# Kernel optimization log

Hardware: AMD Instinct MI355X
Metric: run time of the kernel (lower is better)

The kernel has to match this reference:

```python
import jax, jax.numpy as jnp
import numpy as np

B, S, D = 4, 2048, 768   # batch, seq_len, dim_inp
H, E = 12, 64            # num_heads, dim_out (per-head)
LN_EPS = 1e-5


def setup_inputs() -> dict:
    key = jax.random.key(0)
    ks = jax.random.split(key, 12)
    sd = 1.0 / np.sqrt(D)
    x = jax.random.normal(ks[0], (B, S, D), dtype=jnp.float32)
    Wq = jax.random.normal(ks[1], (H, D, E), dtype=jnp.float32) * sd
    bq = jax.random.normal(ks[2], (H, E), dtype=jnp.float32) * 0.02
    Wk = jax.random.normal(ks[3], (H, D, E), dtype=jnp.float32) * sd
    bk = jax.random.normal(ks[4], (H, E), dtype=jnp.float32) * 0.02
    Wv = jax.random.normal(ks[5], (H, D, E), dtype=jnp.float32) * sd
    bv = jax.random.normal(ks[6], (H, E), dtype=jnp.float32) * 0.02
    Wo = jax.random.normal(ks[7], (H * E, D), dtype=jnp.float32) * (1.0 / np.sqrt(H * E))
    bo = jax.random.normal(ks[8], (D,), dtype=jnp.float32) * 0.02
    gamma = jnp.ones((D,), dtype=jnp.float32)
    beta = jnp.zeros((D,), dtype=jnp.float32)
    return {"input_tensor": x, "Wq": Wq, "bq": bq, "Wk": Wk, "bk": bk,
            "Wv": Wv, "bv": bv, "Wo": Wo, "bo": bo, "gamma": gamma, "beta": beta}


def reference(input_tensor, Wq, bq, Wk, bk, Wv, bv, Wo, bo, gamma, beta):
    x = input_tensor  # [B,S,D]
    # all heads at once: [B,H,S,E]
    q = jnp.einsum('bsd,hde->bhse', x, Wq) + bq[None, :, None, :]
    k = jnp.einsum('bsd,hde->bhse', x, Wk) + bk[None, :, None, :]
    v = jnp.einsum('bsd,hde->bhse', x, Wv) + bv[None, :, None, :]
    # NOTE: original divides by sqrt(seq_len) (query.size(1)), not sqrt(head_dim)
    scale = jnp.sqrt(jnp.float32(q.shape[2]))
    scores = jnp.einsum('bhse,bhte->bhst', q, k) / scale  # [B,H,S,S]
    attn = jax.nn.softmax(scores, axis=-1)
    ctx = jnp.einsum('bhst,bhte->bhse', attn, v)          # [B,H,S,E]
    # concat heads along last dim: [B,S,H*E]
    ctx = ctx.transpose(0, 2, 1, 3).reshape(x.shape[0], x.shape[1], -1)
    proj = ctx @ Wo + bo                                   # [B,S,D]
    h = x + proj
    mu = jnp.mean(h, axis=-1, keepdims=True)
    var = jnp.mean(jnp.square(h - mu), axis=-1, keepdims=True)
    y = (h - mu) * jax.lax.rsqrt(var + LN_EPS) * gamma + beta
    return y
```

## Files before the change

kernel.cpp:

```cpp
#include <hip/hip_runtime.h>


typedef __bf16 bf16x8 __attribute__((ext_vector_type(8)));
typedef __bf16 bf16x4 __attribute__((ext_vector_type(4)));
typedef float  f32x4  __attribute__((ext_vector_type(4)));
typedef float  f32x16 __attribute__((ext_vector_type(16)));
typedef unsigned u32x4 __attribute__((ext_vector_type(4)));

#define MFMA16(a,b,c) __builtin_amdgcn_mfma_f32_16x16x32_bf16((a),(b),(c),0,0,0)
#define MFMA32(a,b,c) __builtin_amdgcn_mfma_f32_32x32x16_bf16((a),(b),(c),0,0,0)
#define QSCALE2 (0.022097086912079612f * 1.4426950408889634f)

__device__ __forceinline__ void gload16(const void* g, void* l) {
  __builtin_amdgcn_global_load_lds((const __attribute__((address_space(1))) void*)g,
                                   (__attribute__((address_space(3))) void*)l, 16, 0, 0);
}

__global__ __launch_bounds__(256) void pack_kernel(
    const float* __restrict__ x, const float* __restrict__ Wq,
    const float* __restrict__ Wk, const float* __restrict__ Wv,
    const float* __restrict__ Wo,
    __bf16* __restrict__ xb, __bf16* __restrict__ wqkv, __bf16* __restrict__ wot) {
  int tid = blockIdx.x * 256 + threadIdx.x;
  int nth = gridDim.x * 256;
  for (int i = tid; i < 8192 * 768 / 4; i += nth) {
    float4 v = ((const float4*)x)[i];
    bf16x4 o; o[0] = (__bf16)v.x; o[1] = (__bf16)v.y; o[2] = (__bf16)v.z; o[3] = (__bf16)v.w;
    ((bf16x4*)xb)[i] = o;
  }
  for (int i = tid; i < 3 * 768 * 768; i += nth) {
    int n = i / 768, d = i - n * 768;
    int p = n / 768;
    int wn = n - p * 768;
    int h = wn >> 6, e = wn & 63;
    const float* W = (p == 0) ? Wq : (p == 1) ? Wk : Wv;
    wqkv[i] = (__bf16)W[(h * 768 + d) * 64 + e];
  }
  for (int i = tid; i < 768 * 768; i += nth) {
    int n = i / 768, k = i - n * 768;
    wot[i] = (__bf16)Wo[k * 768 + n];
  }
}

#define GEMM_CORE(A_, Bt_, m0_, n0_)                                              \
  __shared__ __align__(16) __bf16 As[128 * 64];                                   \
  __shared__ __align__(16) __bf16 Bs[128 * 64];                                   \
  const int tid = threadIdx.x;                                                    \
  const int w = tid >> 6, lane = tid & 63, ln = lane & 15, hi = lane >> 4;        \
  const int wr = w >> 1, wc = w & 1;                                              \
  f32x4 acc[4][4];                                                                \
  {                                                                               \
    f32x4 z = {0.f, 0.f, 0.f, 0.f};                                               \
    _Pragma("unroll") for (int i = 0; i < 4; ++i)                                 \
      _Pragma("unroll") for (int j = 0; j < 4; ++j) acc[i][j] = z;                \
  }                                                                               \
  const int colx0 = ((hi) ^ (ln & 7)) << 4;         \
  const int colx1 = ((4 + hi) ^ (ln & 7)) << 4;     \
  {                                                                               \
    const int r0 = tid >> 3;                       \
    const int scb = ((tid & 7) * 16) ^ ((r0 & 7) << 4);     \
    const char* gA = (const char*)(A_) + (size_t)(m0_ + r0) * 1536 + scb;         \
    const char* gB = (const char*)(Bt_) + (size_t)(n0_ + r0) * 1536 + scb;        \
    char* lA = (char*)As + w * 1024;    \
    char* lB = (char*)Bs + w * 1024;                                              \
    for (int kt = 0; kt < 12; ++kt) {                                             \
      const int kb = kt * 128;                                                    \
      _Pragma("unroll") for (int j = 0; j < 4; ++j) {                             \
        gload16(gA + j * 49152 + kb, lA + j * 4096);                              \
        gload16(gB + j * 49152 + kb, lB + j * 4096);                              \
      }                                                                           \
      __syncthreads();                                                            \
      _Pragma("unroll") for (int kk = 0; kk < 2; ++kk) {                          \
        const int cx = kk ? colx1 : colx0;                                        \
        bf16x8 af[4], bfv[4];                                                     \
        _Pragma("unroll") for (int mt = 0; mt < 4; ++mt)                          \
          af[mt] = *(const bf16x8*)((char*)As + (wr * 64 + mt * 16 + ln) * 128 + cx); \
        _Pragma("unroll") for (int nt = 0; nt < 4; ++nt)                          \
          bfv[nt] = *(const bf16x8*)((char*)Bs + (wc * 64 + nt * 16 + ln) * 128 + cx); \
        _Pragma("unroll") for (int mt = 0; mt < 4; ++mt)                          \
          _Pragma("unroll") for (int nt = 0; nt < 4; ++nt)                        \
            acc[mt][nt] = MFMA16(af[mt], bfv[nt], acc[mt][nt]);                   \
      }                                                                           \
      __syncthreads();                                                            \
    }                                                                             \
  }

__global__ __launch_bounds__(256) void gemm_qkv(
    const __bf16* __restrict__ A, const __bf16* __restrict__ Bt,
    const float* __restrict__ bq, const float* __restrict__ bk,
    const float* __restrict__ bv,
    __bf16* __restrict__ qb, __bf16* __restrict__ kb, __bf16* __restrict__ vt) {
  const int lin = blockIdx.y * 18 + blockIdx.x;
  const int swzb = (lin & 7) * 144 + (lin >> 3);
  const int m0 = (swzb / 18) * 128, n0 = (swzb % 18) * 128;
  GEMM_CORE(A, Bt, m0, n0)
  const int p = n0 / 768;
  const float* bias = (p == 0) ? bq : (p == 1) ? bk : bv;
  const float sc = (p == 0) ? QSCALE2 : 1.0f;
#pragma unroll
  for (int nt = 0; nt < 4; ++nt) {
    int n = n0 + wc * 64 + nt * 16 + ln;
    int wn = n - p * 768;
    int h = wn >> 6, e = wn & 63;
    float bb = bias[wn];
#pragma unroll
    for (int mt = 0; mt < 4; ++mt) {
      int mrow = m0 + wr * 64 + mt * 16 + hi * 4;
      int b = mrow >> 11, s0 = mrow & 2047;
      if (p == 2) {
        bf16x4 pk;
#pragma unroll
        for (int r = 0; r < 4; ++r) pk[r] = (__bf16)(acc[mt][nt][r] + bb);
        *(bf16x4*)&vt[(((size_t)b * 12 + h) * 64 + e) * 2048 + s0] = pk;
      } else {
        __bf16* dst = (p == 0) ? qb : kb;
#pragma unroll
        for (int r = 0; r < 4; ++r)
          dst[(((size_t)b * 12 + h) * 2048 + s0 + r) * 64 + e] =
              (__bf16)((acc[mt][nt][r] + bb) * sc);
      }
    }
  }
}

__global__ __launch_bounds__(256) void gemm_proj(
    const __bf16* __restrict__ A, const __bf16* __restrict__ Bt,
    const float* __restrict__ bo, const __bf16* __restrict__ xres,
    __bf16* __restrict__ hout) {
  const int lin = blockIdx.y * 6 + blockIdx.x;
  const int swzb = (lin & 7) * 48 + (lin >> 3);
  const int m0 = (swzb / 6) * 128, n0 = (swzb % 6) * 128;
  GEMM_CORE(A, Bt, m0, n0)
#pragma unroll
  for (int nt = 0; nt < 4; ++nt) {
    int n = n0 + wc * 64 + nt * 16 + ln;
    float bb = bo[n];
#pragma unroll
    for (int mt = 0; mt < 4; ++mt) {
      int mrow = m0 + wr * 64 + mt * 16 + hi * 4;
#pragma unroll
      for (int r = 0; r < 4; ++r) {
        size_t idx = (size_t)(mrow + r) * 768 + n;
        hout[idx] = (__bf16)(acc[mt][nt][r] + bb + (float)xres[idx]);
      }
    }
  }
}

__global__ __launch_bounds__(256, 3) void attn_kernel(
    const __bf16* __restrict__ qb, const __bf16* __restrict__ kb,
    const __bf16* __restrict__ vt, __bf16* __restrict__ ctx) {
  __shared__ __align__(16) char lds[32768];
  const int tid = threadIdx.x;
  const int w = tid >> 6, lane = tid & 63;
  const int l31 = lane & 31, h = lane >> 5;
  const int bh = blockIdx.x;
  const int q0 = blockIdx.y * 128 + w * 32;

  const int o0 = tid * 16, o1 = o0 + 4096;
  const int r0s = o0 >> 7, cb0 = o0 & 127;
  const int r1s = o1 >> 7, cb1 = o1 & 127;
  const char* kgb = (const char*)(kb + (size_t)bh * 2048 * 64);
  const char* vgb = (const char*)(vt + (size_t)bh * 64 * 2048);
  const char* ksrc0 = kgb + r0s * 128 + (cb0 ^ ((r0s & 7) << 4));
  const char* ksrc1 = kgb + r1s * 128 + (cb1 ^ ((r1s & 7) << 4));
  const char* vsrc0 = vgb + r0s * 4096 + (cb0 ^ ((r0s & 7) << 4));
  const char* vsrc1 = vgb + r1s * 4096 + (cb1 ^ ((r1s & 7) << 4));
  char* kl0 = lds + w * 1024;
  char* vl0 = lds + 16384 + w * 1024;

#define STAGE(t_, b_) do {                                   \
    gload16(ksrc0 + (size_t)(t_) * 8192, kl0 + (b_) * 8192); \
    gload16(ksrc1 + (size_t)(t_) * 8192, kl0 + (b_) * 8192 + 4096); \
    gload16(vsrc0 + (size_t)(t_) * 128,  vl0 + (b_) * 8192); \
    gload16(vsrc1 + (size_t)(t_) * 128,  vl0 + (b_) * 8192 + 4096); \
  } while (0)

  const __bf16* qp = qb + ((size_t)bh * 2048 + q0 + l31) * 64 + h * 8;
  bf16x8 qf[4];
#pragma unroll
  for (int s = 0; s < 4; ++s) qf[s] = *(const bf16x8*)(qp + 16 * s);

  const int swz = (l31 & 7) << 4;
  const int krd = l31 * 128 + ((h * 16) ^ swz);
  const int vrd = 16384 + l31 * 128 + ((h * 16) ^ swz);
  int ka_[8], va_[8];
#pragma unroll
  for (int kvt = 0; kvt < 2; ++kvt)
#pragma unroll
    for (int s = 0; s < 4; ++s) ka_[kvt * 4 + s] = (krd + kvt * 4096) ^ (s * 32);
#pragma unroll
  for (int ks = 0; ks < 4; ++ks)
#pragma unroll
    for (int et = 0; et < 2; ++et) va_[ks * 2 + et] = (vrd + et * 4096) ^ (ks * 32);

  f32x16 FZ;
#pragma unroll
  for (int r = 0; r < 16; ++r) FZ[r] = 0.f;
  bf16x8 onesf;
#pragma unroll
  for (int j = 0; j < 8; ++j) onesf[j] = (__bf16)1.0f;

  f32x16 lacc = FZ;
  f32x16 cacc[2];
  cacc[0] = FZ; cacc[1] = FZ;

  STAGE(0, 0);
  __syncthreads();

#define PKPAIR(dst_, i_)                                                       \
  {                                                                            \
    float pa_ = __builtin_amdgcn_exp2f(sa[2 * (i_)]);                          \
    float pb_ = __builtin_amdgcn_exp2f(sa[2 * (i_) + 1]);                      \
    asm("v_cvt_pk_bf16_f32 %0, %1, %2" : "=v"(dst_) : "v"(pa_), "v"(pb_));     \
  }

#define TILEBODY(B_, T_)                                                       \
  {                                                                            \
    if ((T_) < 31) STAGE((T_) + 1, (B_) ^ 1);                                  \
    bf16x8 kf[2][4], vf[4][2];                                                 \
    _Pragma("unroll") for (int kvt = 0; kvt < 2; ++kvt)                        \
      _Pragma("unroll") for (int s = 0; s < 4; ++s)                            \
        kf[kvt][s] = *(const bf16x8*)(lds + (B_) * 8192 + ka_[kvt * 4 + s]);   \
    _Pragma("unroll") for (int ks = 0; ks < 4; ++ks)                           \
      _Pragma("unroll") for (int et = 0; et < 2; ++et)                         \
        vf[ks][et] = *(const bf16x8*)(lds + (B_) * 8192 + va_[ks * 2 + et]);   \
    u32x4 pau[4];                                                              \
    _Pragma("unroll") for (int kvt = 0; kvt < 2; ++kvt) {                      \
      __builtin_amdgcn_s_setprio(1);                                           \
      f32x16 sa = MFMA32(kf[kvt][0], qf[0], FZ);                               \
      sa = MFMA32(kf[kvt][1], qf[1], sa);                                      \
      sa = MFMA32(kf[kvt][2], qf[2], sa);                                      \
      sa = MFMA32(kf[kvt][3], qf[3], sa);                                      \
      __builtin_amdgcn_s_setprio(0);                                           \
      unsigned c0, c1, c2, c3, c4, c5, c6, c7;                                 \
      PKPAIR(c0, 0) PKPAIR(c1, 1) PKPAIR(c2, 2) PKPAIR(c3, 3)                  \
      PKPAIR(c4, 4) PKPAIR(c5, 5) PKPAIR(c6, 6) PKPAIR(c7, 7)                  \
      asm("v_permlane32_swap_b32 %0, %1" : "+v"(c0), "+v"(c2));                \
      asm("v_permlane32_swap_b32 %0, %1" : "+v"(c1), "+v"(c3));                \
      asm("v_permlane32_swap_b32 %0, %1" : "+v"(c4), "+v"(c6));                \
      asm("v_permlane32_swap_b32 %0, %1" : "+v"(c5), "+v"(c7));                \
      pau[2 * kvt][0] = c0; pau[2 * kvt][1] = c1;                              \
      pau[2 * kvt][2] = c2; pau[2 * kvt][3] = c3;                              \
      pau[2 * kvt + 1][0] = c4; pau[2 * kvt + 1][1] = c5;                      \
      pau[2 * kvt + 1][2] = c6; pau[2 * kvt + 1][3] = c7;                      \
      lacc = MFMA32(__builtin_bit_cast(bf16x8, pau[2 * kvt]), onesf, lacc);    \
      lacc = MFMA32(__builtin_bit_cast(bf16x8, pau[2 * kvt + 1]), onesf, lacc);\
    }                                                                          \
    __builtin_amdgcn_s_setprio(1);                                             \
    _Pragma("unroll") for (int ks = 0; ks < 4; ++ks) {                         \
      bf16x8 paf = __builtin_bit_cast(bf16x8, pau[ks]);                        \
      cacc[0] = MFMA32(paf, vf[ks][0], cacc[0]);                               \
      cacc[1] = MFMA32(paf, vf[ks][1], cacc[1]);                               \
    }                                                                          \
    __builtin_amdgcn_s_setprio(0);                                             \
    __syncthreads();                                                           \
  }

  for (int t = 0; t < 32; t += 2) {
    TILEBODY(0, t)
    TILEBODY(1, t + 1)
  }
#undef TILEBODY
#undef PKPAIR
#undef STAGE

  const int b = bh / 12, hh = bh - b * 12;
#pragma unroll
  for (int r = 0; r < 16; ++r) {
    const int ql = (r & 3) + 8 * (r >> 2) + 4 * h;
    float rl = __builtin_amdgcn_rcpf(lacc[r]);
    size_t base = ((size_t)b * 2048 + q0 + ql) * 768 + hh * 64 + l31;
    ctx[base]      = (__bf16)(cacc[0][r] * rl);
    ctx[base + 32] = (__bf16)(cacc[1][r] * rl);
  }
}

__global__ __launch_bounds__(256) void ln_kernel(
    const __bf16* __restrict__ hb, const float* __restrict__ gamma,
    const float* __restrict__ beta, float* __restrict__ out) {
  __shared__ float ssum[4], ssq[4];
  const int row = blockIdx.x, t = threadIdx.x;
  const __bf16* hr = hb + (size_t)row * 768;
  float v0 = (float)hr[t], v1 = (float)hr[t + 256], v2 = (float)hr[t + 512];
  float sum = v0 + v1 + v2;
  float sq = v0 * v0 + v1 * v1 + v2 * v2;
#pragma unroll
  for (int mask = 1; mask < 64; mask <<= 1) {
    sum += __shfl_xor(sum, mask, 64);
    sq += __shfl_xor(sq, mask, 64);
  }
  const int w = t >> 6;
  if ((t & 63) == 0) { ssum[w] = sum; ssq[w] = sq; }
  __syncthreads();
  float s1 = ssum[0] + ssum[1] + ssum[2] + ssum[3];
  float s2 = ssq[0] + ssq[1] + ssq[2] + ssq[3];
  float mu = s1 * (1.0f / 768.0f);
  float var = s2 * (1.0f / 768.0f) - mu * mu;
  float rs = rsqrtf(var + 1e-5f);
  float* orow = out + (size_t)row * 768;
  orow[t]       = (v0 - mu) * rs * gamma[t]       + beta[t];
  orow[t + 256] = (v1 - mu) * rs * gamma[t + 256] + beta[t + 256];
  orow[t + 512] = (v2 - mu) * rs * gamma[t + 512] + beta[t + 512];
}

extern "C" void kernel_launch(void* const* d_in, const int* in_sizes, int n_in,
                              void* d_out, int out_size, void* d_ws, size_t ws_size,
                              hipStream_t stream) {
  const float* x     = (const float*)d_in[0];
  const float* Wq    = (const float*)d_in[1];
  const float* bq    = (const float*)d_in[2];
  const float* Wk    = (const float*)d_in[3];
  const float* bk    = (const float*)d_in[4];
  const float* Wv    = (const float*)d_in[5];
  const float* bv    = (const float*)d_in[6];
  const float* Wo    = (const float*)d_in[7];
  const float* bo    = (const float*)d_in[8];
  const float* gamma = (const float*)d_in[9];
  const float* beta  = (const float*)d_in[10];
  float* out = (float*)d_out;

  char* ws = (char*)d_ws;
  __bf16* xb   = (__bf16*)(ws);
  __bf16* wqkv = (__bf16*)(ws + 12582912);
  __bf16* wot  = (__bf16*)(ws + 16121856);
  __bf16* qb   = (__bf16*)(ws + 17301504);
  __bf16* kb   = (__bf16*)(ws + 29884416);
  __bf16* vt   = (__bf16*)(ws + 42467328);
  __bf16* ctx  = (__bf16*)(ws + 55050240);
  __bf16* hb   = (__bf16*)(ws + 67633152);

  pack_kernel<<<dim3(1024), dim3(256), 0, stream>>>(x, Wq, Wk, Wv, Wo, xb, wqkv, wot);
  gemm_qkv<<<dim3(18, 64), dim3(256), 0, stream>>>(xb, wqkv, bq, bk, bv, qb, kb, vt);
  attn_kernel<<<dim3(48, 16), dim3(256), 0, stream>>>(qb, kb, vt, ctx);
  gemm_proj<<<dim3(6, 64), dim3(256), 0, stream>>>(ctx, wot, bo, xb, hb);
  ln_kernel<<<dim3(8192), dim3(256), 0, stream>>>(hb, gamma, beta, out);
}
```

Before: 158.1 us.

## Double-buffer GEMM K-tiles and widen attention KV tiles to 128

The shared GEMM core now double-buffers its A/B LDS tiles, issuing the next K-tile's global-to-LDS loads before computing on the current one, so each step needs one barrier instead of two. The attention kernel stages 128 keys per tile instead of 64 and processes each tile as two 64-key halves. This halves the number of barriers and stage rounds over the KV sequence. In exchange, LDS per block doubles: the GEMM goes to 64KB and attention to 64KB with the min-blocks-per-CU hint dropped, which may reduce occupancy.

```diff
diff --git a/kernel.cpp b/kernel.cpp
--- a/kernel.cpp
+++ b/kernel.cpp
@@ -42,9 +42,34 @@
   }
 }
 
+#define GEMM_STEP(B_, T_)                                                         \
+  {                                                                               \
+    if ((T_) < 11) {                                                              \
+      const int kb_ = ((T_) + 1) * 128;                                           \
+      _Pragma("unroll") for (int j = 0; j < 4; ++j) {                             \
+        gload16(gA + j * 49152 + kb_, lA + ((B_) ^ 1) * 16384 + j * 4096);        \
+        gload16(gB + j * 49152 + kb_, lB + ((B_) ^ 1) * 16384 + j * 4096);        \
+      }                                                                           \
+    }                                                                             \
+    _Pragma("unroll") for (int kk = 0; kk < 2; ++kk) {                            \
+      const int cx = kk ? colx1 : colx0;                                          \
+      bf16x8 af[4], bfv[4];                                                       \
+      _Pragma("unroll") for (int mt = 0; mt < 4; ++mt)                            \
+        af[mt] = *(const bf16x8*)((char*)As + (B_) * 16384 +                      \
+                                  (wr * 64 + mt * 16 + ln) * 128 + cx);           \
+      _Pragma("unroll") for (int nt = 0; nt < 4; ++nt)                            \
+        bfv[nt] = *(const bf16x8*)((char*)Bs + (B_) * 16384 +                     \
+                                   (wc * 64 + nt * 16 + ln) * 128 + cx);          \
+      _Pragma("unroll") for (int mt = 0; mt < 4; ++mt)                            \
+        _Pragma("unroll") for (int nt = 0; nt < 4; ++nt)                          \
+          acc[mt][nt] = MFMA16(af[mt], bfv[nt], acc[mt][nt]);                     \
+    }                                                                             \
+    __syncthreads();                                                              \
+  }
+
 #define GEMM_CORE(A_, Bt_, m0_, n0_)                                              \
-  __shared__ __align__(16) __bf16 As[128 * 64];                                   \
-  __shared__ __align__(16) __bf16 Bs[128 * 64];                                   \
+  __shared__ __align__(16) __bf16 As[2][128 * 64];                                \
+  __shared__ __align__(16) __bf16 Bs[2][128 * 64];                                \
   const int tid = threadIdx.x;                                                    \
   const int w = tid >> 6, lane = tid & 63, ln = lane & 15, hi = lane >> 4;        \
   const int wr = w >> 1, wc = w & 1;                                              \
@@ -63,25 +88,14 @@
     const char* gB = (const char*)(Bt_) + (size_t)(n0_ + r0) * 1536 + scb;        \
     char* lA = (char*)As + w * 1024;    \
     char* lB = (char*)Bs + w * 1024;                                              \
-    for (int kt = 0; kt < 12; ++kt) {                                             \
-      const int kb = kt * 128;                                                    \
-      _Pragma("unroll") for (int j = 0; j < 4; ++j) {                             \
-        gload16(gA + j * 49152 + kb, lA + j * 4096);                              \
-        gload16(gB + j * 49152 + kb, lB + j * 4096);                              \
-      }                                                                           \
-      __syncthreads();                                                            \
-      _Pragma("unroll") for (int kk = 0; kk < 2; ++kk) {                          \
-        const int cx = kk ? colx1 : colx0;                                        \
-        bf16x8 af[4], bfv[4];                                                     \
-        _Pragma("unroll") for (int mt = 0; mt < 4; ++mt)                          \
-          af[mt] = *(const bf16x8*)((char*)As + (wr * 64 + mt * 16 + ln) * 128 + cx); \
-        _Pragma("unroll") for (int nt = 0; nt < 4; ++nt)                          \
-          bfv[nt] = *(const bf16x8*)((char*)Bs + (wc * 64 + nt * 16 + ln) * 128 + cx); \
-        _Pragma("unroll") for (int mt = 0; mt < 4; ++mt)                          \
-          _Pragma("unroll") for (int nt = 0; nt < 4; ++nt)                        \
-            acc[mt][nt] = MFMA16(af[mt], bfv[nt], acc[mt][nt]);                   \
-      }                                                                           \
-      __syncthreads();                                                            \
+    _Pragma("unroll") for (int j = 0; j < 4; ++j) {                               \
+      gload16(gA + j * 49152, lA + j * 4096);                                     \
+      gload16(gB + j * 49152, lB + j * 4096);                                     \
+    }                                                                             \
+    __syncthreads();                                                              \
+    for (int kt = 0; kt < 12; kt += 2) {                                          \
+      GEMM_STEP(0, kt)                                                            \
+      GEMM_STEP(1, kt + 1)                                                        \
     }                                                                             \
   }
 
@@ -147,10 +161,10 @@
   }
 }
 
-__global__ __launch_bounds__(256, 3) void attn_kernel(
+__global__ __launch_bounds__(256) void attn_kernel(
     const __bf16* __restrict__ qb, const __bf16* __restrict__ kb,
     const __bf16* __restrict__ vt, __bf16* __restrict__ ctx) {
-  __shared__ __align__(16) char lds[32768];
+  __shared__ __align__(16) char lds[65536];
   const int tid = threadIdx.x;
   const int w = tid >> 6, lane = tid & 63;
   const int l31 = lane & 31, h = lane >> 5;
@@ -167,13 +181,19 @@
   const char* vsrc0 = vgb + r0s * 4096 + (cb0 ^ ((r0s & 7) << 4));
   const char* vsrc1 = vgb + r1s * 4096 + (cb1 ^ ((r1s & 7) << 4));
   char* kl0 = lds + w * 1024;
-  char* vl0 = lds + 16384 + w * 1024;
-
-#define STAGE(t_, b_) do {                                   \
-    gload16(ksrc0 + (size_t)(t_) * 8192, kl0 + (b_) * 8192); \
-    gload16(ksrc1 + (size_t)(t_) * 8192, kl0 + (b_) * 8192 + 4096); \
-    gload16(vsrc0 + (size_t)(t_) * 128,  vl0 + (b_) * 8192); \
-    gload16(vsrc1 + (size_t)(t_) * 128,  vl0 + (b_) * 8192 + 4096); \
+  char* vl0 = lds + 32768 + w * 1024;
+
+#define STAGE128(t_, b_) do {                                                  \
+    char* kd_ = kl0 + (b_) * 16384;                                            \
+    char* vd_ = vl0 + (b_) * 16384;                                            \
+    gload16(ksrc0 + (size_t)(t_) * 16384,        kd_);                         \
+    gload16(ksrc1 + (size_t)(t_) * 16384,        kd_ + 4096);                  \
+    gload16(ksrc0 + (size_t)(t_) * 16384 + 8192, kd_ + 8192);                  \
+    gload16(ksrc1 + (size_t)(t_) * 16384 + 8192, kd_ + 12288);                 \
+    gload16(vsrc0 + (size_t)(t_) * 256,          vd_);                         \
+    gload16(vsrc1 + (size_t)(t_) * 256,          vd_ + 4096);                  \
+    gload16(vsrc0 + (size_t)(t_) * 256 + 128,    vd_ + 8192);                  \
+    gload16(vsrc1 + (size_t)(t_) * 256 + 128,    vd_ + 12288);                 \
   } while (0)
 
   const __bf16* qp = qb + ((size_t)bh * 2048 + q0 + l31) * 64 + h * 8;
@@ -183,7 +203,6 @@
 
   const int swz = (l31 & 7) << 4;
   const int krd = l31 * 128 + ((h * 16) ^ swz);
-  const int vrd = 16384 + l31 * 128 + ((h * 16) ^ swz);
   int ka_[8], va_[8];
 #pragma unroll
   for (int kvt = 0; kvt < 2; ++kvt)
@@ -192,7 +211,7 @@
 #pragma unroll
   for (int ks = 0; ks < 4; ++ks)
 #pragma unroll
-    for (int et = 0; et < 2; ++et) va_[ks * 2 + et] = (vrd + et * 4096) ^ (ks * 32);
+    for (int et = 0; et < 2; ++et) va_[ks * 2 + et] = (krd + et * 4096) ^ (ks * 32);
 
   f32x16 FZ;
 #pragma unroll
@@ -205,7 +224,7 @@
   f32x16 cacc[2];
   cacc[0] = FZ; cacc[1] = FZ;
 
-  STAGE(0, 0);
+  STAGE128(0, 0);
   __syncthreads();
 
 #define PKPAIR(dst_, i_)                                                       \
@@ -215,16 +234,17 @@
     asm("v_cvt_pk_bf16_f32 %0, %1, %2" : "=v"(dst_) : "v"(pa_), "v"(pb_));     \
   }
 
-#define TILEBODY(B_, T_)                                                       \
+#define TILEHALF(KB_, VB_)                                                     \
   {                                                                            \
-    if ((T_) < 31) STAGE((T_) + 1, (B_) ^ 1);                                  \
+    const char* kb_l = (KB_);                                                  \
+    const char* vb_l = (VB_);                                                  \
     bf16x8 kf[2][4], vf[4][2];                                                 \
     _Pragma("unroll") for (int kvt = 0; kvt < 2; ++kvt)                        \
       _Pragma("unroll") for (int s = 0; s < 4; ++s)                            \
-        kf[kvt][s] = *(const bf16x8*)(lds + (B_) * 8192 + ka_[kvt * 4 + s]);   \
+        kf[kvt][s] = *(const bf16x8*)(kb_l + ka_[kvt * 4 + s]);                \
     _Pragma("unroll") for (int ks = 0; ks < 4; ++ks)                           \
       _Pragma("unroll") for (int et = 0; et < 2; ++et)                         \
-        vf[ks][et] = *(const bf16x8*)(lds + (B_) * 8192 + va_[ks * 2 + et]);   \
+        vf[ks][et] = *(const bf16x8*)(vb_l + va_[ks * 2 + et]);                \
     u32x4 pau[4];                                                              \
     _Pragma("unroll") for (int kvt = 0; kvt < 2; ++kvt) {                      \
       __builtin_amdgcn_s_setprio(1);                                           \
@@ -254,16 +274,24 @@
       cacc[1] = MFMA32(paf, vf[ks][1], cacc[1]);                               \
     }                                                                          \
     __builtin_amdgcn_s_setprio(0);                                             \
+  }
+
+#define TILE128(B_, T_)                                                        \
+  {                                                                            \
+    if ((T_) < 15) STAGE128((T_) + 1, (B_) ^ 1);                               \
+    TILEHALF(lds + (B_) * 16384,        lds + 32768 + (B_) * 16384)            \
+    TILEHALF(lds + (B_) * 16384 + 8192, lds + 32768 + (B_) * 16384 + 8192)     \
     __syncthreads();                                                           \
   }
 
-  for (int t = 0; t < 32; t += 2) {
-    TILEBODY(0, t)
-    TILEBODY(1, t + 1)
-  }
-#undef TILEBODY
+  for (int t = 0; t < 16; t += 2) {
+    TILE128(0, t)
+    TILE128(1, t + 1)
+  }
+#undef TILE128
+#undef TILEHALF
 #undef PKPAIR
-#undef STAGE
+#undef STAGE128
 
   const int b = bh / 12, hh = bh - b * 12;
 #pragma unroll
```

Result: slower. 171.3 us (+8.4%).

## Split attention KV range in two blocks and merge partials in combine kernel

Applied to the files above, without the earlier changes.

Each attention block now handles half of the key/value sequence, doubling the grid to 48x32 blocks. Unnormalized partial contexts and row sums go to workspace, and a new combine kernel adds the two halves and divides by the summed denominator. Row sums are now accumulated with scalar adds and a cross-lane shuffle instead of an extra MFMA against a ones vector, and launch bounds request 4 blocks per CU. The intent is better occupancy and wave count on the GPU, at the cost of extra global traffic for the partial results, one more kernel launch, and bf16 rounding of the partials before they are combined.

```diff
diff --git a/kernel.cpp b/kernel.cpp
--- a/kernel.cpp
+++ b/kernel.cpp
@@ -147,21 +147,24 @@
   }
 }
 
-__global__ __launch_bounds__(256, 3) void attn_kernel(
+__global__ __launch_bounds__(256, 4) void attn_kernel(
     const __bf16* __restrict__ qb, const __bf16* __restrict__ kb,
-    const __bf16* __restrict__ vt, __bf16* __restrict__ ctx) {
+    const __bf16* __restrict__ vt, __bf16* __restrict__ pc,
+    float* __restrict__ pl) {
   __shared__ __align__(16) char lds[32768];
   const int tid = threadIdx.x;
   const int w = tid >> 6, lane = tid & 63;
   const int l31 = lane & 31, h = lane >> 5;
   const int bh = blockIdx.x;
-  const int q0 = blockIdx.y * 128 + w * 32;
+  const int yy = blockIdx.y;
+  const int half = yy & 1;
+  const int q0 = (yy >> 1) * 128 + w * 32;
 
   const int o0 = tid * 16, o1 = o0 + 4096;
   const int r0s = o0 >> 7, cb0 = o0 & 127;
   const int r1s = o1 >> 7, cb1 = o1 & 127;
-  const char* kgb = (const char*)(kb + (size_t)bh * 2048 * 64);
-  const char* vgb = (const char*)(vt + (size_t)bh * 64 * 2048);
+  const char* kgb = (const char*)(kb + (size_t)bh * 2048 * 64) + half * 131072;
+  const char* vgb = (const char*)(vt + (size_t)bh * 64 * 2048) + half * 2048;
   const char* ksrc0 = kgb + r0s * 128 + (cb0 ^ ((r0s & 7) << 4));
   const char* ksrc1 = kgb + r1s * 128 + (cb1 ^ ((r1s & 7) << 4));
   const char* vsrc0 = vgb + r0s * 4096 + (cb0 ^ ((r0s & 7) << 4));
@@ -197,27 +200,25 @@
   f32x16 FZ;
 #pragma unroll
   for (int r = 0; r < 16; ++r) FZ[r] = 0.f;
-  bf16x8 onesf;
-#pragma unroll
-  for (int j = 0; j < 8; ++j) onesf[j] = (__bf16)1.0f;
-
-  f32x16 lacc = FZ;
+
+  float ls0 = 0.f, ls1 = 0.f, ls2 = 0.f, ls3 = 0.f;
   f32x16 cacc[2];
   cacc[0] = FZ; cacc[1] = FZ;
 
   STAGE(0, 0);
   __syncthreads();
 
-#define PKPAIR(dst_, i_)                                                       \
+#define PKPAIR(dst_, i_, ls_)                                                  \
   {                                                                            \
     float pa_ = __builtin_amdgcn_exp2f(sa[2 * (i_)]);                          \
     float pb_ = __builtin_amdgcn_exp2f(sa[2 * (i_) + 1]);                      \
+    ls_ += pa_ + pb_;                                                          \
     asm("v_cvt_pk_bf16_f32 %0, %1, %2" : "=v"(dst_) : "v"(pa_), "v"(pb_));     \
   }
 
 #define TILEBODY(B_, T_)                                                       \
   {                                                                            \
-    if ((T_) < 31) STAGE((T_) + 1, (B_) ^ 1);                                  \
+    if ((T_) < 15) STAGE((T_) + 1, (B_) ^ 1);                                  \
     bf16x8 kf[2][4], vf[4][2];                                                 \
     _Pragma("unroll") for (int kvt = 0; kvt < 2; ++kvt)                        \
       _Pragma("unroll") for (int s = 0; s < 4; ++s)                            \
@@ -234,8 +235,8 @@
       sa = MFMA32(kf[kvt][3], qf[3], sa);                                      \
       __builtin_amdgcn_s_setprio(0);                                           \
       unsigned c0, c1, c2, c3, c4, c5, c6, c7;                                 \
-      PKPAIR(c0, 0) PKPAIR(c1, 1) PKPAIR(c2, 2) PKPAIR(c3, 3)                  \
-      PKPAIR(c4, 4) PKPAIR(c5, 5) PKPAIR(c6, 6) PKPAIR(c7, 7)                  \
+      PKPAIR(c0, 0, ls0) PKPAIR(c1, 1, ls1) PKPAIR(c2, 2, ls2) PKPAIR(c3, 3, ls3) \
+      PKPAIR(c4, 4, ls0) PKPAIR(c5, 5, ls1) PKPAIR(c6, 6, ls2) PKPAIR(c7, 7, ls3) \
       asm("v_permlane32_swap_b32 %0, %1" : "+v"(c0), "+v"(c2));                \
       asm("v_permlane32_swap_b32 %0, %1" : "+v"(c1), "+v"(c3));                \
       asm("v_permlane32_swap_b32 %0, %1" : "+v"(c4), "+v"(c6));                \
@@ -244,8 +245,6 @@
       pau[2 * kvt][2] = c2; pau[2 * kvt][3] = c3;                              \
       pau[2 * kvt + 1][0] = c4; pau[2 * kvt + 1][1] = c5;                      \
       pau[2 * kvt + 1][2] = c6; pau[2 * kvt + 1][3] = c7;                      \
-      lacc = MFMA32(__builtin_bit_cast(bf16x8, pau[2 * kvt]), onesf, lacc);    \
-      lacc = MFMA32(__builtin_bit_cast(bf16x8, pau[2 * kvt + 1]), onesf, lacc);\
     }                                                                          \
     __builtin_amdgcn_s_setprio(1);                                             \
     _Pragma("unroll") for (int ks = 0; ks < 4; ++ks) {                         \
@@ -257,7 +256,7 @@
     __syncthreads();                                                           \
   }
 
-  for (int t = 0; t < 32; t += 2) {
+  for (int t = 0; t < 16; t += 2) {
     TILEBODY(0, t)
     TILEBODY(1, t + 1)
   }
@@ -265,15 +264,38 @@
 #undef PKPAIR
 #undef STAGE
 
+  float lsum = (ls0 + ls1) + (ls2 + ls3);
+  lsum += __shfl_xor(lsum, 32, 64);
+  __bf16* pcH = pc + (size_t)half * 6291456;
+  float* plH = pl + half * 98304;
   const int b = bh / 12, hh = bh - b * 12;
+  if (h == 0) plH[bh * 2048 + q0 + l31] = lsum;
 #pragma unroll
   for (int r = 0; r < 16; ++r) {
     const int ql = (r & 3) + 8 * (r >> 2) + 4 * h;
-    float rl = __builtin_amdgcn_rcpf(lacc[r]);
     size_t base = ((size_t)b * 2048 + q0 + ql) * 768 + hh * 64 + l31;
-    ctx[base]      = (__bf16)(cacc[0][r] * rl);
-    ctx[base + 32] = (__bf16)(cacc[1][r] * rl);
-  }
+    pcH[base]      = (__bf16)cacc[0][r];
+    pcH[base + 32] = (__bf16)cacc[1][r];
+  }
+}
+
+__global__ __launch_bounds__(256) void combine_kernel(
+    const __bf16* __restrict__ pc, const float* __restrict__ pl,
+    __bf16* __restrict__ ctx) {
+  const int i = blockIdx.x * 256 + threadIdx.x;
+  const int base = i * 4;
+  const int row = base / 768;
+  const int c = base - row * 768;
+  const int b = row >> 11, q = row & 2047, h = c >> 6;
+  const int lidx = ((b * 12 + h) << 11) + q;
+  const float den = pl[lidx] + pl[98304 + lidx];
+  const float rl = __builtin_amdgcn_rcpf(den);
+  bf16x4 a = *(const bf16x4*)(pc + base);
+  bf16x4 d = *(const bf16x4*)(pc + 6291456 + base);
+  bf16x4 o;
+#pragma unroll
+  for (int j = 0; j < 4; ++j) o[j] = (__bf16)(((float)a[j] + (float)d[j]) * rl);
+  *(bf16x4*)(ctx + base) = o;
 }
 
 __global__ __launch_bounds__(256) void ln_kernel(
@@ -329,10 +351,13 @@
   __bf16* vt   = (__bf16*)(ws + 42467328);
   __bf16* ctx  = (__bf16*)(ws + 55050240);
   __bf16* hb   = (__bf16*)(ws + 67633152);
+  __bf16* pc   = (__bf16*)(ws + 67633152);
+  float*  pl   = (float*)(ws + 92798976);
 
   pack_kernel<<<dim3(1024), dim3(256), 0, stream>>>(x, Wq, Wk, Wv, Wo, xb, wqkv, wot);
   gemm_qkv<<<dim3(18, 64), dim3(256), 0, stream>>>(xb, wqkv, bq, bk, bv, qb, kb, vt);
-  attn_kernel<<<dim3(48, 16), dim3(256), 0, stream>>>(qb, kb, vt, ctx);
+  attn_kernel<<<dim3(48, 32), dim3(256), 0, stream>>>(qb, kb, vt, pc, pl);
+  combine_kernel<<<dim3(6144), dim3(256), 0, stream>>>(pc, pl, ctx);
   gemm_proj<<<dim3(6, 64), dim3(256), 0, stream>>>(ctx, wot, bo, xb, hb);
   ln_kernel<<<dim3(8192), dim3(256), 0, stream>>>(hb, gamma, beta, out);
 }
```

Result: slower. 284.2 us (+79.8%).
